# Kernel optimization log

Measured on AMD Instinct MI355X. Metric: run time of the kernel, lower is better.

## Reference

```python
import jax, jax.numpy as jnp
import numpy as np

B, H, W, C = 4, 64, 64, 256
DQK = C // 16  # query/key channels = 16


def setup_inputs() -> dict:
    key = jax.random.key(0)
    ks = jax.random.split(key, 8)
    s = 0.05
    return {
        "x": jax.random.normal(ks[0], (B, H, W, C), dtype=jnp.float32),
        "wq": jax.random.normal(ks[1], (C, DQK), dtype=jnp.float32) * s,
        "bq": jax.random.normal(ks[2], (DQK,), dtype=jnp.float32) * s,
        "wk": jax.random.normal(ks[3], (C, DQK), dtype=jnp.float32) * s,
        "bk": jax.random.normal(ks[4], (DQK,), dtype=jnp.float32) * s,
        "wv": jax.random.normal(ks[5], (C, C), dtype=jnp.float32) * s,
        "bv": jax.random.normal(ks[6], (C,), dtype=jnp.float32) * s,
        "gamma": jax.random.normal(ks[7], (), dtype=jnp.float32),
    }


def reference(x, wq, bq, wk, bk, wv, bv, gamma):
    # 1x1 convs == per-pixel linear projections
    q = jnp.einsum('bhwc,cd->bhwd', x, wq) + bq          # [B,H,W,DQK]
    k = jnp.einsum('bhwc,cd->bhwd', x, wk) + bk          # [B,H,W,DQK]
    v = jnp.einsum('bhwc,cd->bhwd', x, wv) + bv          # [B,H,W,C]
    hw = H * W
    q = q.reshape(B, hw, DQK)
    k = k.reshape(B, hw, DQK)
    v = v.reshape(B, hw, C)
    energy = jnp.einsum('bnd,bmd->bnm', q, k)            # [B,HW,HW]
    attention = jax.nn.softmax(energy, axis=-1)
    out = jnp.einsum('bnm,bmc->bnc', attention, v)       # [B,HW,C]
    out = out.reshape(B, H, W, C)
    return out * gamma + x, attention
```

## Files before the change

kernel.cpp:

```cpp
#include <hip/hip_runtime.h>

typedef _Float16 half8 __attribute__((ext_vector_type(8)));
typedef _Float16 half4v __attribute__((ext_vector_type(4)));
typedef __fp16 fp16x2 __attribute__((ext_vector_type(2)));
typedef float f32x16 __attribute__((ext_vector_type(16)));
typedef unsigned int uint2v __attribute__((ext_vector_type(2)));

#define MFMA16(a, b, c) __builtin_amdgcn_mfma_f32_32x32x16_f16((a), (b), (c), 0, 0, 0)

#define OFF_WB   0
#define OFF_WQK  131072
#define OFF_QF   147456
#define OFF_KF   671744
#define OFF_VB   1196032

__device__ inline unsigned int pkf16(float a, float b) {
    union { fp16x2 h; unsigned int u; } cv;
    cv.h = __builtin_amdgcn_cvt_pkrtz(a, b);
    return cv.u;
}
__device__ inline half8 mk8(unsigned int w0, unsigned int w1, unsigned int w2, unsigned int w3) {
    union { unsigned int u[4]; half8 h; } cv;
    cv.u[0] = w0; cv.u[1] = w1; cv.u[2] = w2; cv.u[3] = w3; return cv.h;
}

__global__ __launch_bounds__(256) void k_prep(const float* __restrict__ wq,
                                              const float* __restrict__ wk,
                                              const float* __restrict__ wv,
                                              _Float16* __restrict__ WB,
                                              _Float16* __restrict__ WQK) {
    int idx = blockIdx.x * 256 + threadIdx.x;
    if (idx < 65536) {
        int j = idx & 7, l = (idx >> 3) & 63, kc = idx >> 12;
        int ct = (idx >> 9) & 7;
        int k = kc * 16 + (l >> 5) * 8 + j;
        int c = ct * 32 + (l & 31);
        WB[idx] = (_Float16)wv[k * 256 + c];
    } else if (idx < 65536 + 8192) {
        int t = idx - 65536;
        int j = t & 7, l = (t >> 3) & 63, kc = t >> 9;
        int k = kc * 16 + (l >> 5) * 8 + j;
        int c = l & 31;
        WQK[t] = (_Float16)((c < 16) ? wq[k * 16 + c] : wk[k * 16 + (c - 16)]);
    }
}

__global__ __launch_bounds__(256, 2) void k_proj(const float* __restrict__ x,
                                                 const float* __restrict__ bq,
                                                 const float* __restrict__ bk,
                                                 const float* __restrict__ bv,
                                                 const _Float16* __restrict__ WB,
                                                 const _Float16* __restrict__ WQK,
                                                 _Float16* __restrict__ Qf,
                                                 _Float16* __restrict__ Kf,
                                                 _Float16* __restrict__ VB) {
    const int tid = threadIdx.x;
    const int w = tid >> 6, l = tid & 63, lo = l & 31, h = l >> 5;
    const long rowbase = (long)blockIdx.x * 32;
    const float* xp = x + (rowbase + lo) * 256 + h * 8;

    f32x16 acc0 = {}, acc1 = {}, accQK = {};
#pragma unroll
    for (int kc = 0; kc < 16; ++kc) {
        float4 a0 = *(const float4*)(xp + kc * 16);
        float4 a1 = *(const float4*)(xp + kc * 16 + 4);
        half8 xf;
        xf[0] = (_Float16)a0.x; xf[1] = (_Float16)a0.y; xf[2] = (_Float16)a0.z; xf[3] = (_Float16)a0.w;
        xf[4] = (_Float16)a1.x; xf[5] = (_Float16)a1.y; xf[6] = (_Float16)a1.z; xf[7] = (_Float16)a1.w;
        half8 b0 = *(const half8*)(WB + ((kc * 8 + 2 * w) * 64 + l) * 8);
        half8 b1 = *(const half8*)(WB + ((kc * 8 + 2 * w + 1) * 64 + l) * 8);
        acc0 = MFMA16(xf, b0, acc0);
        acc1 = MFMA16(xf, b1, acc1);
        if (w == 0) {
            half8 bqk = *(const half8*)(WQK + (kc * 64 + l) * 8);
            accQK = MFMA16(xf, bqk, accQK);
        }
    }

    const int b = (int)(rowbase >> 12);
    const int k16base = (int)((rowbase & 4095) >> 4);
#pragma unroll
    for (int cti = 0; cti < 2; ++cti) {
        int ct = 2 * w + cti;
        f32x16 acc = cti ? acc1 : acc0;
        float bias = bv[ct * 32 + lo];
#pragma unroll
        for (int g = 0; g < 4; ++g) {
            int K16 = k16base + (g >> 1);
            int lanep = (g & 1) * 32 + lo;
            _Float16* dst = VB + ((((long)b * 256 + K16) * 8 + ct) * 64 + lanep) * 8 + 4 * h;
            half4v pv;
            pv[0] = (_Float16)(acc[4 * g + 0] + bias);
            pv[1] = (_Float16)(acc[4 * g + 1] + bias);
            pv[2] = (_Float16)(acc[4 * g + 2] + bias);
            pv[3] = (_Float16)(acc[4 * g + 3] + bias);
            *(half4v*)dst = pv;
        }
    }
    if (w == 0) {
        float bias = (lo < 16) ? bq[lo] : bk[lo - 16];
#pragma unroll
        for (int r = 0; r < 16; ++r) {
            int kl = (r & 3) + 8 * (r >> 2) + 4 * h;
            long n = rowbase + kl;
            _Float16 val = (_Float16)(accQK[r] + bias);
            if (lo < 16) Qf[n * 16 + lo] = val;
            else         Kf[n * 16 + (lo - 16)] = val;
        }
    }
}

__global__ __launch_bounds__(256, 2) void k_attn(const float* __restrict__ x,
                                                 const float* __restrict__ gptr,
                                                 const _Float16* __restrict__ Qf,
                                                 const _Float16* __restrict__ Kf,
                                                 const _Float16* __restrict__ VB,
                                                 float* __restrict__ out0,
                                                 float* __restrict__ attn) {
    const int bid = blockIdx.x;
    const int xcd = bid & 7, sslot = bid >> 3;
    const int b = xcd >> 1;
    const int qt = (xcd & 1) * 64 + sslot;
    const int tid = threadIdx.x, w = tid >> 6, l = tid & 63, lo = l & 31, h = l >> 5;
    const int qbase = qt * 32;

    half8 qf = *(const half8*)(Qf + (((long)b * 4096 + qbase + lo) << 4) + h * 8);
    const _Float16* Kb = Kf + ((long)b * 4096 << 4);

    float m = -3e38f, lsum = 0.f;
    for (int i = 0; i < 32; ++i) {
        int t = i * 4 + w;
        half8 kf = *(const half8*)(Kb + ((t * 32 + lo) << 4) + h * 8);
        f32x16 e = MFMA16(kf, qf, (f32x16){});
        float tmax = e[0];
#pragma unroll
        for (int r = 1; r < 16; ++r) tmax = fmaxf(tmax, e[r]);
        tmax = fmaxf(tmax, __shfl_xor(tmax, 32));
        float mn = fmaxf(m, tmax);
        float sc = __expf(m - mn);
        float ss = 0.f;
#pragma unroll
        for (int r = 0; r < 16; ++r) ss += __expf(e[r] - mn);
        lsum = lsum * sc + ss;
        m = mn;
    }
    lsum += __shfl_xor(lsum, 32);

    __shared__ float sm[4][32];
    __shared__ float sl[4][32];
    if (l < 32) { sm[w][lo] = m; sl[w][lo] = lsum; }
    __syncthreads();
    float M = fmaxf(fmaxf(sm[0][lo], sm[1][lo]), fmaxf(sm[2][lo], sm[3][lo]));
    float L = sl[0][lo] * __expf(sm[0][lo] - M) + sl[1][lo] * __expf(sm[1][lo] - M) +
              sl[2][lo] * __expf(sm[2][lo] - M) + sl[3][lo] * __expf(sm[3][lo] - M);
    float rl = 1.0f / L;

    float* Arow = attn + (long)b * 4096 * 4096 + (long)(qbase + lo) * 4096;
    const _Float16* vb = VB + (long)b * 256 * 8 * 64 * 8;
    f32x16 oacc[8] = {};

    for (int i = 0; i < 32; ++i) {
        int t = i * 4 + w;
        half8 kf = *(const half8*)(Kb + ((t * 32 + lo) << 4) + h * 8);
        f32x16 e = MFMA16(kf, qf, (f32x16){});
        float p[16];
#pragma unroll
        for (int r = 0; r < 16; ++r) p[r] = __expf(e[r] - M) * rl;

        float* ap = Arow + t * 32 + 4 * h;
#pragma unroll
        for (int g = 0; g < 4; ++g) {
            float4 st = { p[4 * g], p[4 * g + 1], p[4 * g + 2], p[4 * g + 3] };
            *(float4*)(ap + 8 * g) = st;
        }

        unsigned int u0 = pkf16(p[0], p[1]),   x0 = pkf16(p[4], p[5]);
        unsigned int v0 = pkf16(p[2], p[3]),   y0 = pkf16(p[6], p[7]);
        unsigned int u1 = pkf16(p[8], p[9]),   x1 = pkf16(p[12], p[13]);
        unsigned int v1 = pkf16(p[10], p[11]), y1 = pkf16(p[14], p[15]);
        uint2v t0 = __builtin_amdgcn_permlane32_swap(u0, x0, false, false);
        uint2v t1 = __builtin_amdgcn_permlane32_swap(v0, y0, false, false);
        uint2v t2 = __builtin_amdgcn_permlane32_swap(u1, x1, false, false);
        uint2v t3 = __builtin_amdgcn_permlane32_swap(v1, y1, false, false);
        half8 pa0 = mk8(t0.x, t1.x, t0.y, t1.y);
        half8 pa1 = mk8(t2.x, t3.x, t2.y, t3.y);

#pragma unroll
        for (int ct = 0; ct < 8; ++ct) {
            half8 vf0 = *(const half8*)(vb + (((long)(2 * t + 0) * 8 + ct) * 64 + l) * 8);
            half8 vf1 = *(const half8*)(vb + (((long)(2 * t + 1) * 8 + ct) * 64 + l) * 8);
            oacc[ct] = MFMA16(pa0, vf0, oacc[ct]);
            oacc[ct] = MFMA16(pa1, vf1, oacc[ct]);
        }
    }

    __shared__ float ldsO[32][256];
#pragma unroll 1
    for (int ww = 0; ww < 4; ++ww) {
        if (w == ww) {
#pragma unroll
            for (int ct = 0; ct < 8; ++ct) {
#pragma unroll
                for (int r = 0; r < 16; ++r) {
                    int row = (r & 3) + 8 * (r >> 2) + 4 * h;
                    float val = oacc[ct][r];
                    if (ww == 0) ldsO[row][ct * 32 + lo] = val;
                    else         ldsO[row][ct * 32 + lo] += val;
                }
            }
        }
        __syncthreads();
    }

    float gamma = *gptr;
    int row = tid >> 3;
    int cb = (tid & 7) << 5;
    long base = ((long)b * 4096 + qbase + row) * 256 + cb;
    const float* xp = x + base;
    float* op = out0 + base;
#pragma unroll
    for (int c0 = 0; c0 < 32; c0 += 4) {
        float4 xv = *(const float4*)(xp + c0);
        float4 ov;
        ov.x = gamma * ldsO[row][cb + c0 + 0] + xv.x;
        ov.y = gamma * ldsO[row][cb + c0 + 1] + xv.y;
        ov.z = gamma * ldsO[row][cb + c0 + 2] + xv.z;
        ov.w = gamma * ldsO[row][cb + c0 + 3] + xv.w;
        *(float4*)(op + c0) = ov;
    }
}

extern "C" void kernel_launch(void* const* d_in, const int* in_sizes, int n_in,
                              void* d_out, int out_size, void* d_ws, size_t ws_size,
                              hipStream_t stream) {
    const float* x  = (const float*)d_in[0];
    const float* wq = (const float*)d_in[1];
    const float* bq = (const float*)d_in[2];
    const float* wk = (const float*)d_in[3];
    const float* bk = (const float*)d_in[4];
    const float* wv = (const float*)d_in[5];
    const float* bv = (const float*)d_in[6];
    const float* gamma = (const float*)d_in[7];

    char* ws = (char*)d_ws;
    _Float16* WB  = (_Float16*)(ws + OFF_WB);
    _Float16* WQK = (_Float16*)(ws + OFF_WQK);
    _Float16* Qf  = (_Float16*)(ws + OFF_QF);
    _Float16* Kf  = (_Float16*)(ws + OFF_KF);
    _Float16* VB  = (_Float16*)(ws + OFF_VB);

    float* out0 = (float*)d_out;
    float* attn = (float*)d_out + 4194304;

    k_prep<<<288, 256, 0, stream>>>(wq, wk, wv, WB, WQK);
    k_proj<<<512, 256, 0, stream>>>(x, bq, bk, bv, WB, WQK, Qf, Kf, VB);
    k_attn<<<512, 256, 0, stream>>>(x, gamma, Qf, Kf, VB, out0, attn);
}
```

Measured before the change: 146.9 us.

## Split softmax stats into separate kernels and split attention over channel halves

```diff
diff --git a/kernel.cpp b/kernel.cpp
--- a/kernel.cpp
+++ b/kernel.cpp
@@ -4,15 +4,19 @@
 typedef _Float16 half4v __attribute__((ext_vector_type(4)));
 typedef __fp16 fp16x2 __attribute__((ext_vector_type(2)));
 typedef float f32x16 __attribute__((ext_vector_type(16)));
+typedef float f32x4 __attribute__((ext_vector_type(4)));
 typedef unsigned int uint2v __attribute__((ext_vector_type(2)));
 
 #define MFMA16(a, b, c) __builtin_amdgcn_mfma_f32_32x32x16_f16((a), (b), (c), 0, 0, 0)
+#define QSC 1.44269504088896f
 
 #define OFF_WB   0
 #define OFF_WQK  131072
 #define OFF_QF   147456
 #define OFF_KF   671744
 #define OFF_VB   1196032
+#define OFF_MLP  9584640
+#define OFF_S    9846784
 
 __device__ inline unsigned int pkf16(float a, float b) {
     union { fp16x2 h; unsigned int u; } cv;
@@ -103,61 +107,92 @@
         for (int r = 0; r < 16; ++r) {
             int kl = (r & 3) + 8 * (r >> 2) + 4 * h;
             long n = rowbase + kl;
-            _Float16 val = (_Float16)(accQK[r] + bias);
-            if (lo < 16) Qf[n * 16 + lo] = val;
-            else         Kf[n * 16 + (lo - 16)] = val;
-        }
-    }
-}
-
-__global__ __launch_bounds__(256, 2) void k_attn(const float* __restrict__ x,
+            float v = accQK[r] + bias;
+            if (lo < 16) Qf[n * 16 + lo] = (_Float16)(v * QSC);
+            else         Kf[n * 16 + (lo - 16)] = (_Float16)v;
+        }
+    }
+}
+
+__global__ __launch_bounds__(256, 4) void k_ml(const _Float16* __restrict__ Qf,
+                                               const _Float16* __restrict__ Kf,
+                                               float2* __restrict__ MLp) {
+    const int bid = blockIdx.x;
+    const int kh = bid & 1;
+    const int qi = bid >> 1;
+    const int b = qi >> 7, qt = qi & 127;
+    const int tid = threadIdx.x, w = tid >> 6, l = tid & 63, lo = l & 31, h = l >> 5;
+    const int qbase = qt * 32;
+
+    half8 qf = *(const half8*)(Qf + (((long)b * 4096 + qbase + lo) << 4) + h * 8);
+    const _Float16* Kb = Kf + ((long)b * 4096 << 4);
+
+    float m = -3e38f, lsum = 0.f;
+    for (int i = 0; i < 16; ++i) {
+        int t = kh * 64 + i * 4 + w;
+        half8 kf = *(const half8*)(Kb + ((t * 32 + lo) << 4) + h * 8);
+        f32x16 e = MFMA16(kf, qf, (f32x16){});
+        float t0 = fmaxf(fmaxf(e[0], e[1]), fmaxf(e[2], e[3]));
+        float t1 = fmaxf(fmaxf(e[4], e[5]), fmaxf(e[6], e[7]));
+        float t2 = fmaxf(fmaxf(e[8], e[9]), fmaxf(e[10], e[11]));
+        float t3 = fmaxf(fmaxf(e[12], e[13]), fmaxf(e[14], e[15]));
+        float tmax = fmaxf(fmaxf(t0, t1), fmaxf(t2, t3));
+        tmax = fmaxf(tmax, __shfl_xor(tmax, 32));
+        if (tmax > m) { lsum *= exp2f(m - tmax); m = tmax; }
+        float ss = 0.f;
+#pragma unroll
+        for (int r = 0; r < 16; ++r) ss += exp2f(e[r] - m);
+        lsum += ss;
+    }
+    lsum += __shfl_xor(lsum, 32);
+
+    __shared__ float sm[4][32];
+    __shared__ float sl[4][32];
+    if (l < 32) { sm[w][lo] = m; sl[w][lo] = lsum; }
+    __syncthreads();
+    if (tid < 32) {
+        float M = fmaxf(fmaxf(sm[0][tid], sm[1][tid]), fmaxf(sm[2][tid], sm[3][tid]));
+        float L = sl[0][tid] * exp2f(sm[0][tid] - M) + sl[1][tid] * exp2f(sm[1][tid] - M) +
+                  sl[2][tid] * exp2f(sm[2][tid] - M) + sl[3][tid] * exp2f(sm[3][tid] - M);
+        float2 v; v.x = M; v.y = L;
+        MLp[(((long)b * 4096 + qbase + tid) << 1) + kh] = v;
+    }
+}
+
+__global__ __launch_bounds__(256) void k_ml2(const float2* __restrict__ MLp,
+                                             float* __restrict__ S) {
+    int idx = blockIdx.x * 256 + threadIdx.x;
+    float2 a = MLp[idx * 2 + 0];
+    float2 c = MLp[idx * 2 + 1];
+    float M = fmaxf(a.x, c.x);
+    float L = a.y * exp2f(a.x - M) + c.y * exp2f(c.x - M);
+    S[idx] = M + __log2f(L);
+}
+
+__global__ __launch_bounds__(256, 3) void k_attn(const float* __restrict__ x,
                                                  const float* __restrict__ gptr,
                                                  const _Float16* __restrict__ Qf,
                                                  const _Float16* __restrict__ Kf,
                                                  const _Float16* __restrict__ VB,
+                                                 const float* __restrict__ Sbuf,
                                                  float* __restrict__ out0,
                                                  float* __restrict__ attn) {
     const int bid = blockIdx.x;
-    const int xcd = bid & 7, sslot = bid >> 3;
+    const int xcd = bid & 7, slot = bid >> 3;
     const int b = xcd >> 1;
-    const int qt = (xcd & 1) * 64 + sslot;
+    const int qt = (xcd & 1) * 64 + (slot & 63);
+    const int ch = slot >> 6;
     const int tid = threadIdx.x, w = tid >> 6, l = tid & 63, lo = l & 31, h = l >> 5;
     const int qbase = qt * 32;
 
     half8 qf = *(const half8*)(Qf + (((long)b * 4096 + qbase + lo) << 4) + h * 8);
     const _Float16* Kb = Kf + ((long)b * 4096 << 4);
-
-    float m = -3e38f, lsum = 0.f;
-    for (int i = 0; i < 32; ++i) {
-        int t = i * 4 + w;
-        half8 kf = *(const half8*)(Kb + ((t * 32 + lo) << 4) + h * 8);
-        f32x16 e = MFMA16(kf, qf, (f32x16){});
-        float tmax = e[0];
-#pragma unroll
-        for (int r = 1; r < 16; ++r) tmax = fmaxf(tmax, e[r]);
-        tmax = fmaxf(tmax, __shfl_xor(tmax, 32));
-        float mn = fmaxf(m, tmax);
-        float sc = __expf(m - mn);
-        float ss = 0.f;
-#pragma unroll
-        for (int r = 0; r < 16; ++r) ss += __expf(e[r] - mn);
-        lsum = lsum * sc + ss;
-        m = mn;
-    }
-    lsum += __shfl_xor(lsum, 32);
-
-    __shared__ float sm[4][32];
-    __shared__ float sl[4][32];
-    if (l < 32) { sm[w][lo] = m; sl[w][lo] = lsum; }
-    __syncthreads();
-    float M = fmaxf(fmaxf(sm[0][lo], sm[1][lo]), fmaxf(sm[2][lo], sm[3][lo]));
-    float L = sl[0][lo] * __expf(sm[0][lo] - M) + sl[1][lo] * __expf(sm[1][lo] - M) +
-              sl[2][lo] * __expf(sm[2][lo] - M) + sl[3][lo] * __expf(sm[3][lo] - M);
-    float rl = 1.0f / L;
-
+    const float S_lane = Sbuf[b * 4096 + qbase + lo];
+    const _Float16* vb = VB + (long)b * 256 * 8 * 64 * 8;
     float* Arow = attn + (long)b * 4096 * 4096 + (long)(qbase + lo) * 4096;
-    const _Float16* vb = VB + (long)b * 256 * 8 * 64 * 8;
-    f32x16 oacc[8] = {};
+    const int g0 = 2 * ch;
+
+    f32x16 oacc[4] = {};
 
     for (int i = 0; i < 32; ++i) {
         int t = i * 4 + w;
@@ -165,14 +200,13 @@
         f32x16 e = MFMA16(kf, qf, (f32x16){});
         float p[16];
 #pragma unroll
-        for (int r = 0; r < 16; ++r) p[r] = __expf(e[r] - M) * rl;
+        for (int r = 0; r < 16; ++r) p[r] = exp2f(e[r] - S_lane);
 
         float* ap = Arow + t * 32 + 4 * h;
-#pragma unroll
-        for (int g = 0; g < 4; ++g) {
-            float4 st = { p[4 * g], p[4 * g + 1], p[4 * g + 2], p[4 * g + 3] };
-            *(float4*)(ap + 8 * g) = st;
-        }
+        f32x4 s0 = { p[4 * g0 + 0], p[4 * g0 + 1], p[4 * g0 + 2], p[4 * g0 + 3] };
+        f32x4 s1 = { p[4 * g0 + 4], p[4 * g0 + 5], p[4 * g0 + 6], p[4 * g0 + 7] };
+        __builtin_nontemporal_store(s0, (f32x4*)(ap + 8 * g0));
+        __builtin_nontemporal_store(s1, (f32x4*)(ap + 8 * g0 + 8));
 
         unsigned int u0 = pkf16(p[0], p[1]),   x0 = pkf16(p[4], p[5]);
         unsigned int v0 = pkf16(p[2], p[3]),   y0 = pkf16(p[6], p[7]);
@@ -186,20 +220,21 @@
         half8 pa1 = mk8(t2.x, t3.x, t2.y, t3.y);
 
 #pragma unroll
-        for (int ct = 0; ct < 8; ++ct) {
-            half8 vf0 = *(const half8*)(vb + (((long)(2 * t + 0) * 8 + ct) * 64 + l) * 8);
-            half8 vf1 = *(const half8*)(vb + (((long)(2 * t + 1) * 8 + ct) * 64 + l) * 8);
+        for (int ct = 0; ct < 4; ++ct) {
+            int ctg = 4 * ch + ct;
+            half8 vf0 = *(const half8*)(vb + (((long)(2 * t + 0) * 8 + ctg) * 64 + l) * 8);
+            half8 vf1 = *(const half8*)(vb + (((long)(2 * t + 1) * 8 + ctg) * 64 + l) * 8);
             oacc[ct] = MFMA16(pa0, vf0, oacc[ct]);
             oacc[ct] = MFMA16(pa1, vf1, oacc[ct]);
         }
     }
 
-    __shared__ float ldsO[32][256];
+    __shared__ float ldsO[32][128];
 #pragma unroll 1
     for (int ww = 0; ww < 4; ++ww) {
         if (w == ww) {
 #pragma unroll
-            for (int ct = 0; ct < 8; ++ct) {
+            for (int ct = 0; ct < 4; ++ct) {
 #pragma unroll
                 for (int r = 0; r < 16; ++r) {
                     int row = (r & 3) + 8 * (r >> 2) + 4 * h;
@@ -214,19 +249,19 @@
 
     float gamma = *gptr;
     int row = tid >> 3;
-    int cb = (tid & 7) << 5;
-    long base = ((long)b * 4096 + qbase + row) * 256 + cb;
+    int cb = (tid & 7) << 4;
+    long base = ((long)b * 4096 + qbase + row) * 256 + ch * 128 + cb;
     const float* xp = x + base;
     float* op = out0 + base;
 #pragma unroll
-    for (int c0 = 0; c0 < 32; c0 += 4) {
+    for (int c0 = 0; c0 < 16; c0 += 4) {
         float4 xv = *(const float4*)(xp + c0);
-        float4 ov;
+        f32x4 ov;
         ov.x = gamma * ldsO[row][cb + c0 + 0] + xv.x;
         ov.y = gamma * ldsO[row][cb + c0 + 1] + xv.y;
         ov.z = gamma * ldsO[row][cb + c0 + 2] + xv.z;
         ov.w = gamma * ldsO[row][cb + c0 + 3] + xv.w;
-        *(float4*)(op + c0) = ov;
+        __builtin_nontemporal_store(ov, (f32x4*)(op + c0));
     }
 }
 
@@ -248,11 +283,15 @@
     _Float16* Qf  = (_Float16*)(ws + OFF_QF);
     _Float16* Kf  = (_Float16*)(ws + OFF_KF);
     _Float16* VB  = (_Float16*)(ws + OFF_VB);
+    float2*   MLp = (float2*)(ws + OFF_MLP);
+    float*    S   = (float*)(ws + OFF_S);
 
     float* out0 = (float*)d_out;
     float* attn = (float*)d_out + 4194304;
 
     k_prep<<<288, 256, 0, stream>>>(wq, wk, wv, WB, WQK);
     k_proj<<<512, 256, 0, stream>>>(x, bq, bk, bv, WB, WQK, Qf, Kf, VB);
-    k_attn<<<512, 256, 0, stream>>>(x, gamma, Qf, Kf, VB, out0, attn);
-}
+    k_ml  <<<1024, 256, 0, stream>>>(Qf, Kf, MLp);
+    k_ml2 <<<64, 256, 0, stream>>>(MLp, S);
+    k_attn<<<1024, 256, 0, stream>>>(x, gamma, Qf, Kf, VB, S, out0, attn);
+}
```

Result: slower. 225.9 us (+53.8%).
